# Kernel optimization log

Measured on AMD Instinct MI355X. Metric: run time of the kernel, lower is better.

Reference implementation:

```python
import jax, jax.numpy as jnp
import numpy as np
from jax import lax

C = 64
K = 7
HALF = K // 2
SIGMA_MIN = 0.6
SIGMA_MAX = 1.2

_SOBEL_X = jnp.array([[-1., 0., 1.], [-2., 0., 2.], [-1., 0., 1.]], dtype=jnp.float32).reshape(1, 1, 3, 3)
_SOBEL_Y = jnp.transpose(_SOBEL_X, (0, 1, 3, 2))


def _depthwise3x3(x, kern):
    # x: [B,C,H,W]; same 3x3 kernel per channel -> fold C into batch, 1-channel conv
    B, Cc, H, W = x.shape
    y = lax.conv_general_dilated(
        x.reshape(B * Cc, 1, H, W), kern,
        window_strides=(1, 1), padding=((1, 1), (1, 1)),
        dimension_numbers=('NCHW', 'OIHW', 'NCHW'))
    return y.reshape(B, Cc, H, W)


def _shift_stack(xp, W_out, axis):
    # xp padded by HALF along `axis`; stack K shifted views along new last axis
    views = [lax.slice_in_dim(xp, i, i + W_out, axis=axis) for i in range(K)]
    return jnp.stack(views, axis=-1)


def setup_inputs() -> dict:
    key = jax.random.key(0)
    x = jax.random.normal(key, (4, C, 256, 256), dtype=jnp.float32)
    return {"x": x}


def reference(x) -> jnp.ndarray:
    B, Cc, H, W = x.shape
    # Sobel edge magnitude, mean over channels
    gx = _depthwise3x3(x, _SOBEL_X)
    gy = _depthwise3x3(x, _SOBEL_Y)
    edge = (gx ** 2 + gy ** 2).mean(axis=1, keepdims=True)  # [B,1,H,W]
    emin = edge.min(axis=(2, 3), keepdims=True)
    emax = edge.max(axis=(2, 3), keepdims=True)
    edge = (edge - emin) / (emax + 1e-6)  # note: denom = amax + eps (faithful)
    sigma = SIGMA_MIN + (SIGMA_MAX - SIGMA_MIN) * edge  # [B,1,H,W]

    # per-pixel 1D gaussian kernel, shared across channels: [B,1,H,W,K]
    offs = jnp.arange(-HALF, HALF + 1, dtype=x.dtype)
    g = jnp.exp(-(offs ** 2) / (2.0 * sigma[..., None] ** 2))
    g = g / g.sum(axis=-1, keepdims=True)

    # horizontal pass: pad W, gather K shifted views, weighted sum
    xp = jnp.pad(x, ((0, 0), (0, 0), (0, 0), (HALF, HALF)))
    out = (_shift_stack(xp, W, axis=3) * g).sum(axis=-1)
    # vertical pass with the same per-pixel kernel
    op = jnp.pad(out, ((0, 0), (0, 0), (HALF, HALF), (0, 0)))
    out = (_shift_stack(op, H, axis=2) * g).sum(axis=-1)
    return out
```

## Files before the change

### kernel.cpp

```cpp
#include <hip/hip_runtime.h>
#include <cstddef>

namespace {
constexpr int B = 4, C = 64, H = 256, W = 256;
constexpr int HW = H * W;
constexpr int CHW = C * HW;
constexpr int CG = 4;
constexpr int TH = 16;
constexpr float SMIN = 0.6f, SMAX = 1.2f;
typedef float vfloat4 __attribute__((ext_vector_type(4)));
}

__device__ __forceinline__ float4 ld4(const float* p) {
  return *(const float4*)p;
}
__device__ __forceinline__ void st4(float* p, float a, float b, float c, float d) {
  float4 v; v.x = a; v.y = b; v.z = c; v.w = d; *(float4*)p = v;
}
__device__ __forceinline__ void st4nt(float* p, float a, float b, float c, float d) {
  vfloat4 v; v.x = a; v.y = b; v.z = c; v.w = d;
  __builtin_nontemporal_store(v, (vfloat4*)p);
}

__global__ __launch_bounds__(256) void edge_kernel(
    const float* __restrict__ x, float* __restrict__ P) {
  __shared__ float part[4][4][64][4];
  const int xcd = blockIdx.x & 7;
  const int slot = blockIdx.x >> 3;
  const int hbb = slot & 7;
  const int cb = slot >> 3;
  const int h0 = xcd * 32 + hbb * 4;
  const int cg = cb >> 2;
  const int b = cb & 3;
  const int lane = threadIdx.x & 63, wv = threadIdx.x >> 6;
  const float* base = x + (size_t)b * CHW + 4 * lane;
  const int c0 = cg * 16 + wv * 4;
  float acc[4][4] = {};
  #pragma unroll
  for (int cc = 0; cc < 4; ++cc) {
    const float* p = base + (size_t)(c0 + cc) * HW;
    float4 R[6];
    #pragma unroll
    for (int i = 0; i < 6; ++i) {
      const int gh = h0 - 1 + i;
      R[i] = (gh >= 0 && gh < H) ? ld4(p + (size_t)gh * W)
                                 : float4{0.f, 0.f, 0.f, 0.f};
    }
    float Lh[6], Rh[6];
    #pragma unroll
    for (int i = 0; i < 6; ++i) {
      Lh[i] = __shfl_up(R[i].w, 1);
      Rh[i] = __shfl_down(R[i].x, 1);
    }
    if (lane == 0) {
      #pragma unroll
      for (int i = 0; i < 6; ++i) Lh[i] = 0.f;
    }
    if (lane == 63) {
      #pragma unroll
      for (int i = 0; i < 6; ++i) Rh[i] = 0.f;
    }
    #pragma unroll
    for (int r = 0; r < 4; ++r) {
      const float ra[6] = {Lh[r],     R[r].x,     R[r].y,     R[r].z,     R[r].w,     Rh[r]};
      const float rb[6] = {Lh[r + 1], R[r + 1].x, R[r + 1].y, R[r + 1].z, R[r + 1].w, Rh[r + 1]};
      const float rc[6] = {Lh[r + 2], R[r + 2].x, R[r + 2].y, R[r + 2].z, R[r + 2].w, Rh[r + 2]};
      #pragma unroll
      for (int j = 0; j < 4; ++j) {
        float gx = (ra[j + 2] - ra[j]) + 2.f * (rb[j + 2] - rb[j]) + (rc[j + 2] - rc[j]);
        float gy = (rc[j] - ra[j]) + 2.f * (rc[j + 1] - ra[j + 1]) + (rc[j + 2] - ra[j + 2]);
        acc[r][j] = fmaf(gx, gx, acc[r][j]);
        acc[r][j] = fmaf(gy, gy, acc[r][j]);
      }
    }
  }
  #pragma unroll
  for (int r = 0; r < 4; ++r)
    #pragma unroll
    for (int j = 0; j < 4; ++j) part[wv][r][lane][j] = acc[r][j];
  __syncthreads();
  {
    const int r = wv;
    float s[4];
    #pragma unroll
    for (int j = 0; j < 4; ++j)
      s[j] = part[0][r][lane][j] + part[1][r][lane][j] +
             part[2][r][lane][j] + part[3][r][lane][j];
    st4nt(P + (size_t)(cg * B + b) * HW + (size_t)(h0 + r) * W + 4 * lane,
          s[0], s[1], s[2], s[3]);
  }
}

__global__ __launch_bounds__(256) void combine_kernel(
    const float* __restrict__ P, float* __restrict__ edge,
    float* __restrict__ mmp) {
  __shared__ float smn[4], smx[4];
  const int t = blockIdx.x * 256 + threadIdx.x;
  const int pix4 = t * 4;
  const int b = pix4 >> 16;
  const int off = pix4 & (HW - 1);
  float4 s0 = ld4(P + (size_t)(0 * B + b) * HW + off);
  float4 s1 = ld4(P + (size_t)(1 * B + b) * HW + off);
  float4 s2 = ld4(P + (size_t)(2 * B + b) * HW + off);
  float4 s3 = ld4(P + (size_t)(3 * B + b) * HW + off);
  float e0 = (s0.x + s1.x + s2.x + s3.x) * (1.f / 64.f);
  float e1 = (s0.y + s1.y + s2.y + s3.y) * (1.f / 64.f);
  float e2 = (s0.z + s1.z + s2.z + s3.z) * (1.f / 64.f);
  float e3 = (s0.w + s1.w + s2.w + s3.w) * (1.f / 64.f);
  st4(edge + pix4, e0, e1, e2, e3);
  float mn = fminf(fminf(e0, e1), fminf(e2, e3));
  float mx = fmaxf(fmaxf(e0, e1), fmaxf(e2, e3));
  #pragma unroll
  for (int o = 32; o > 0; o >>= 1) {
    mn = fminf(mn, __shfl_down(mn, o, 64));
    mx = fmaxf(mx, __shfl_down(mx, o, 64));
  }
  const int lane = threadIdx.x & 63, wv = threadIdx.x >> 6;
  if (lane == 0) { smn[wv] = mn; smx[wv] = mx; }
  __syncthreads();
  if (threadIdx.x == 0) {
    mn = fminf(fminf(smn[0], smn[1]), fminf(smn[2], smn[3]));
    mx = fmaxf(fmaxf(smx[0], smx[1]), fmaxf(smx[2], smx[3]));
    mmp[2 * (b * 64 + (blockIdx.x & 63))] = mn;
    mmp[2 * (b * 64 + (blockIdx.x & 63)) + 1] = mx;
  }
}

__global__ __launch_bounds__(256) void weights_kernel(
    const float* __restrict__ edge, const float* __restrict__ mmp,
    float* __restrict__ wt) {
  const int t = blockIdx.x * 256 + threadIdx.x;
  const int pix4 = t * 4;
  const int b = pix4 >> 16;
  const int lane = threadIdx.x & 63;
  float2 mv = *(const float2*)&mmp[2 * (b * 64 + lane)];
  float mn = mv.x, mx = mv.y;
  #pragma unroll
  for (int o = 1; o < 64; o <<= 1) {
    mn = fminf(mn, __shfl_xor(mn, o, 64));
    mx = fmaxf(mx, __shfl_xor(mx, o, 64));
  }
  const float emin = mn;
  const float inv_den = 1.f / (mx + 1e-6f);
  float4 ev = ld4(edge + pix4);
  const float E[4] = {ev.x, ev.y, ev.z, ev.w};
  float r[8];
  #pragma unroll
  for (int j = 0; j < 4; ++j) {
    float en = (E[j] - emin) * inv_den;
    float sg = SMIN + (SMAX - SMIN) * en;
    float a = 1.0f / (2.0f * sg * sg);
    float e1 = __expf(-a);
    float t2 = e1 * e1, e4 = t2 * t2, e9 = e4 * e4 * e1;
    float inv = 1.f / (1.f + 2.f * (e1 + e4 + e9));
    r[2 * j] = e1; r[2 * j + 1] = inv;
  }
  st4(wt + (size_t)pix4 * 2,     r[0], r[1], r[2], r[3]);
  st4(wt + (size_t)pix4 * 2 + 4, r[4], r[5], r[6], r[7]);
}

__device__ __forceinline__ void recon_g(float e1, float inv, float g[7]) {
  float t2 = e1 * e1, e4 = t2 * t2, e9 = e4 * e4 * e1;
  g[3] = inv; g[2] = e1 * inv; g[1] = e4 * inv; g[0] = e9 * inv;
  g[4] = g[2]; g[5] = g[1]; g[6] = g[0];
}

__global__ __launch_bounds__(256) void fusedblur_kernel(
    const float* __restrict__ x, const float* __restrict__ wt,
    float* __restrict__ out) {
  __shared__ float hb[TH + 6][W];
  const int xcd = blockIdx.x & 7;
  const int slot = blockIdx.x >> 3;
  const int s = slot & 15;
  const int bc = xcd * 32 + (slot >> 4);
  const int b = bc >> 6;
  const int h0 = s * TH;
  const int lane = threadIdx.x & 63, wv = threadIdx.x >> 6;
  const float* xp = x + (size_t)bc * HW + 4 * lane;
  const float* wp = wt + (size_t)b * HW * 2 + 8 * lane;
  float* op = out + (size_t)bc * HW + 4 * lane;

  for (int r = wv; r < TH + 6; r += 4) {
    const int gh = h0 - 3 + r;
    float4 o = {0.f, 0.f, 0.f, 0.f};
    if (gh >= 0 && gh < H) {
      float4 v = ld4(xp + (size_t)gh * W);
      float4 q0 = ld4(wp + (size_t)gh * W * 2);
      float4 q1 = ld4(wp + (size_t)gh * W * 2 + 4);
      float L1 = __shfl_up(v.y, 1), L2 = __shfl_up(v.z, 1), L3 = __shfl_up(v.w, 1);
      float R1 = __shfl_down(v.x, 1), R2 = __shfl_down(v.y, 1), R3 = __shfl_down(v.z, 1);
      if (lane == 0)  { L1 = 0.f; L2 = 0.f; L3 = 0.f; }
      if (lane == 63) { R1 = 0.f; R2 = 0.f; R3 = 0.f; }
      const float win[10] = {L1, L2, L3, v.x, v.y, v.z, v.w, R1, R2, R3};
      const float E1[4] = {q0.x, q0.z, q1.x, q1.z};
      const float IV[4] = {q0.y, q0.w, q1.y, q1.w};
      float acc[4];
      #pragma unroll
      for (int j = 0; j < 4; ++j) {
        float g[7]; recon_g(E1[j], IV[j], g);
        float sacc = g[0] * win[j];
        #pragma unroll
        for (int i = 1; i < 7; ++i) sacc = fmaf(g[i], win[j + i], sacc);
        acc[j] = sacc;
      }
      o.x = acc[0]; o.y = acc[1]; o.z = acc[2]; o.w = acc[3];
    }
    *(float4*)&hb[r][4 * lane] = o;
  }
  __syncthreads();

  const int r0 = wv * 4;
  float win7[7][4];
  #pragma unroll
  for (int i = 0; i < 7; ++i) {
    float4 v = *(const float4*)&hb[r0 + i][4 * lane];
    win7[i][0] = v.x; win7[i][1] = v.y; win7[i][2] = v.z; win7[i][3] = v.w;
  }
  #pragma unroll
  for (int k = 0; k < 4; ++k) {
    const int gh = h0 + r0 + k;
    float4 q0 = ld4(wp + (size_t)gh * W * 2);
    float4 q1 = ld4(wp + (size_t)gh * W * 2 + 4);
    const float E1[4] = {q0.x, q0.z, q1.x, q1.z};
    const float IV[4] = {q0.y, q0.w, q1.y, q1.w};
    float acc[4];
    #pragma unroll
    for (int j = 0; j < 4; ++j) {
      float g[7]; recon_g(E1[j], IV[j], g);
      float sacc = g[0] * win7[0][j];
      #pragma unroll
      for (int i = 1; i < 7; ++i) sacc = fmaf(g[i], win7[i][j], sacc);
      acc[j] = sacc;
    }
    st4nt(op + (size_t)gh * W, acc[0], acc[1], acc[2], acc[3]);
    if (k < 3) {
      #pragma unroll
      for (int i = 0; i < 6; ++i) {
        #pragma unroll
        for (int j = 0; j < 4; ++j) win7[i][j] = win7[i + 1][j];
      }
      float4 nv = *(const float4*)&hb[r0 + k + 7][4 * lane];
      win7[6][0] = nv.x; win7[6][1] = nv.y; win7[6][2] = nv.z; win7[6][3] = nv.w;
    }
  }
}

extern "C" void kernel_launch(void* const* d_in, const int* in_sizes, int n_in,
                              void* d_out, int out_size, void* d_ws, size_t ws_size,
                              hipStream_t stream) {
  const float* x = (const float*)d_in[0];
  float* out = (float*)d_out;

  float* mmp = (float*)d_ws;
  float* edge = (float*)((char*)d_ws + 4096);
  float* wt = (float*)((char*)d_ws + 4096 + (size_t)B * HW * 4);
  float* P = (float*)((char*)d_ws + 4096 + (size_t)B * HW * 12);

  edge_kernel<<<B * CG * (H / 4), 256, 0, stream>>>(x, P);
  combine_kernel<<<(B * HW / 4) / 256, 256, 0, stream>>>(P, edge, mmp);
  weights_kernel<<<(B * HW / 4) / 256, 256, 0, stream>>>(edge, mmp, wt);
  fusedblur_kernel<<<B * C * (H / TH), 256, 0, stream>>>(x, wt, out);
}
```

Baseline: 134.7 us.

## Fuse combine and weights kernels with atomic grid-wide min/max barrier

```diff
diff --git a/kernel.cpp b/kernel.cpp
--- a/kernel.cpp
+++ b/kernel.cpp
@@ -5,7 +5,8 @@
 constexpr int B = 4, C = 64, H = 256, W = 256;
 constexpr int HW = H * W;
 constexpr int CHW = C * HW;
-constexpr int CG = 4;
+constexpr int CG = 8;
+constexpr int BH = 8;
 constexpr int TH = 16;
 constexpr float SMIN = 0.6f, SMAX = 1.2f;
 typedef float vfloat4 __attribute__((ext_vector_type(4)));
@@ -21,47 +22,54 @@
   vfloat4 v; v.x = a; v.y = b; v.z = c; v.w = d;
   __builtin_nontemporal_store(v, (vfloat4*)p);
 }
+__device__ __forceinline__ float4 ld4nt(const float* p) {
+  vfloat4 v = __builtin_nontemporal_load((const vfloat4*)p);
+  float4 r; r.x = v.x; r.y = v.y; r.z = v.z; r.w = v.w; return r;
+}
 
 __global__ __launch_bounds__(256) void edge_kernel(
-    const float* __restrict__ x, float* __restrict__ P) {
-  __shared__ float part[4][4][64][4];
+    const float* __restrict__ x, float* __restrict__ P,
+    unsigned int* __restrict__ mm) {
+  __shared__ float part[4][BH][64][4];
+  if (blockIdx.x == 0 && threadIdx.x < 2 * B + 1)
+    mm[threadIdx.x] = (threadIdx.x < B) ? 0x7f7fffffu : 0u;
   const int xcd = blockIdx.x & 7;
   const int slot = blockIdx.x >> 3;
-  const int hbb = slot & 7;
-  const int cb = slot >> 3;
-  const int h0 = xcd * 32 + hbb * 4;
+  const int hbb = slot & 3;
+  const int cb = slot >> 2;
+  const int h0 = xcd * 32 + hbb * BH;
   const int cg = cb >> 2;
   const int b = cb & 3;
   const int lane = threadIdx.x & 63, wv = threadIdx.x >> 6;
   const float* base = x + (size_t)b * CHW + 4 * lane;
-  const int c0 = cg * 16 + wv * 4;
-  float acc[4][4] = {};
-  #pragma unroll
-  for (int cc = 0; cc < 4; ++cc) {
+  const int c0 = cg * 8 + wv * 2;
+  float acc[BH][4] = {};
+  #pragma unroll
+  for (int cc = 0; cc < 2; ++cc) {
     const float* p = base + (size_t)(c0 + cc) * HW;
-    float4 R[6];
-    #pragma unroll
-    for (int i = 0; i < 6; ++i) {
+    float4 R[BH + 2];
+    #pragma unroll
+    for (int i = 0; i < BH + 2; ++i) {
       const int gh = h0 - 1 + i;
       R[i] = (gh >= 0 && gh < H) ? ld4(p + (size_t)gh * W)
                                  : float4{0.f, 0.f, 0.f, 0.f};
     }
-    float Lh[6], Rh[6];
-    #pragma unroll
-    for (int i = 0; i < 6; ++i) {
+    float Lh[BH + 2], Rh[BH + 2];
+    #pragma unroll
+    for (int i = 0; i < BH + 2; ++i) {
       Lh[i] = __shfl_up(R[i].w, 1);
       Rh[i] = __shfl_down(R[i].x, 1);
     }
     if (lane == 0) {
       #pragma unroll
-      for (int i = 0; i < 6; ++i) Lh[i] = 0.f;
+      for (int i = 0; i < BH + 2; ++i) Lh[i] = 0.f;
     }
     if (lane == 63) {
       #pragma unroll
-      for (int i = 0; i < 6; ++i) Rh[i] = 0.f;
-    }
-    #pragma unroll
-    for (int r = 0; r < 4; ++r) {
+      for (int i = 0; i < BH + 2; ++i) Rh[i] = 0.f;
+    }
+    #pragma unroll
+    for (int r = 0; r < BH; ++r) {
       const float ra[6] = {Lh[r],     R[r].x,     R[r].y,     R[r].z,     R[r].w,     Rh[r]};
       const float rb[6] = {Lh[r + 1], R[r + 1].x, R[r + 1].y, R[r + 1].z, R[r + 1].w, Rh[r + 1]};
       const float rc[6] = {Lh[r + 2], R[r + 2].x, R[r + 2].y, R[r + 2].z, R[r + 2].w, Rh[r + 2]};
@@ -75,12 +83,13 @@
     }
   }
   #pragma unroll
-  for (int r = 0; r < 4; ++r)
+  for (int r = 0; r < BH; ++r)
     #pragma unroll
     for (int j = 0; j < 4; ++j) part[wv][r][lane][j] = acc[r][j];
   __syncthreads();
-  {
-    const int r = wv;
+  #pragma unroll
+  for (int rr = 0; rr < 2; ++rr) {
+    const int r = wv + 4 * rr;
     float s[4];
     #pragma unroll
     for (int j = 0; j < 4; ++j)
@@ -91,25 +100,25 @@
   }
 }
 
-__global__ __launch_bounds__(256) void combine_kernel(
-    const float* __restrict__ P, float* __restrict__ edge,
-    float* __restrict__ mmp) {
+__global__ __launch_bounds__(256) void combine_weights_kernel(
+    const float* __restrict__ P, unsigned int* __restrict__ mm,
+    float* __restrict__ wt) {
   __shared__ float smn[4], smx[4];
+  __shared__ unsigned int sld[2];
   const int t = blockIdx.x * 256 + threadIdx.x;
   const int pix4 = t * 4;
   const int b = pix4 >> 16;
   const int off = pix4 & (HW - 1);
-  float4 s0 = ld4(P + (size_t)(0 * B + b) * HW + off);
-  float4 s1 = ld4(P + (size_t)(1 * B + b) * HW + off);
-  float4 s2 = ld4(P + (size_t)(2 * B + b) * HW + off);
-  float4 s3 = ld4(P + (size_t)(3 * B + b) * HW + off);
-  float e0 = (s0.x + s1.x + s2.x + s3.x) * (1.f / 64.f);
-  float e1 = (s0.y + s1.y + s2.y + s3.y) * (1.f / 64.f);
-  float e2 = (s0.z + s1.z + s2.z + s3.z) * (1.f / 64.f);
-  float e3 = (s0.w + s1.w + s2.w + s3.w) * (1.f / 64.f);
-  st4(edge + pix4, e0, e1, e2, e3);
-  float mn = fminf(fminf(e0, e1), fminf(e2, e3));
-  float mx = fmaxf(fmaxf(e0, e1), fmaxf(e2, e3));
+  float e[4] = {};
+  #pragma unroll
+  for (int g = 0; g < CG; ++g) {
+    float4 sv = ld4nt(P + (size_t)(g * B + b) * HW + off);
+    e[0] += sv.x; e[1] += sv.y; e[2] += sv.z; e[3] += sv.w;
+  }
+  #pragma unroll
+  for (int j = 0; j < 4; ++j) e[j] *= (1.f / 64.f);
+  float mn = fminf(fminf(e[0], e[1]), fminf(e[2], e[3]));
+  float mx = fmaxf(fmaxf(e[0], e[1]), fmaxf(e[2], e[3]));
   #pragma unroll
   for (int o = 32; o > 0; o >>= 1) {
     mn = fminf(mn, __shfl_down(mn, o, 64));
@@ -121,33 +130,23 @@
   if (threadIdx.x == 0) {
     mn = fminf(fminf(smn[0], smn[1]), fminf(smn[2], smn[3]));
     mx = fmaxf(fmaxf(smx[0], smx[1]), fmaxf(smx[2], smx[3]));
-    mmp[2 * (b * 64 + (blockIdx.x & 63))] = mn;
-    mmp[2 * (b * 64 + (blockIdx.x & 63)) + 1] = mx;
-  }
-}
-
-__global__ __launch_bounds__(256) void weights_kernel(
-    const float* __restrict__ edge, const float* __restrict__ mmp,
-    float* __restrict__ wt) {
-  const int t = blockIdx.x * 256 + threadIdx.x;
-  const int pix4 = t * 4;
-  const int b = pix4 >> 16;
-  const int lane = threadIdx.x & 63;
-  float2 mv = *(const float2*)&mmp[2 * (b * 64 + lane)];
-  float mn = mv.x, mx = mv.y;
-  #pragma unroll
-  for (int o = 1; o < 64; o <<= 1) {
-    mn = fminf(mn, __shfl_xor(mn, o, 64));
-    mx = fmaxf(mx, __shfl_xor(mx, o, 64));
-  }
-  const float emin = mn;
-  const float inv_den = 1.f / (mx + 1e-6f);
-  float4 ev = ld4(edge + pix4);
-  const float E[4] = {ev.x, ev.y, ev.z, ev.w};
+    atomicMin(mm + b, __float_as_uint(mn));
+    atomicMax(mm + B + b, __float_as_uint(mx));
+    __threadfence();
+    atomicAdd(mm + 2 * B, 1u);
+    while (__hip_atomic_load(mm + 2 * B, __ATOMIC_ACQUIRE,
+                             __HIP_MEMORY_SCOPE_AGENT) < gridDim.x)
+      __builtin_amdgcn_s_sleep(2);
+    sld[0] = __hip_atomic_load(mm + b, __ATOMIC_ACQUIRE, __HIP_MEMORY_SCOPE_AGENT);
+    sld[1] = __hip_atomic_load(mm + B + b, __ATOMIC_ACQUIRE, __HIP_MEMORY_SCOPE_AGENT);
+  }
+  __syncthreads();
+  const float emin = __uint_as_float(sld[0]);
+  const float inv_den = 1.f / (__uint_as_float(sld[1]) + 1e-6f);
   float r[8];
   #pragma unroll
   for (int j = 0; j < 4; ++j) {
-    float en = (E[j] - emin) * inv_den;
+    float en = (e[j] - emin) * inv_den;
     float sg = SMIN + (SMAX - SMIN) * en;
     float a = 1.0f / (2.0f * sg * sg);
     float e1 = __expf(-a);
@@ -251,13 +250,11 @@
   const float* x = (const float*)d_in[0];
   float* out = (float*)d_out;
 
-  float* mmp = (float*)d_ws;
-  float* edge = (float*)((char*)d_ws + 4096);
-  float* wt = (float*)((char*)d_ws + 4096 + (size_t)B * HW * 4);
-  float* P = (float*)((char*)d_ws + 4096 + (size_t)B * HW * 12);
-
-  edge_kernel<<<B * CG * (H / 4), 256, 0, stream>>>(x, P);
-  combine_kernel<<<(B * HW / 4) / 256, 256, 0, stream>>>(P, edge, mmp);
-  weights_kernel<<<(B * HW / 4) / 256, 256, 0, stream>>>(edge, mmp, wt);
+  unsigned int* mm = (unsigned int*)d_ws;
+  float* wt = (float*)((char*)d_ws + 4096);
+  float* P = (float*)((char*)d_ws + 4096 + (size_t)B * HW * 8);
+
+  edge_kernel<<<B * CG * (H / BH), 256, 0, stream>>>(x, P, mm);
+  combine_weights_kernel<<<(B * HW / 4) / 256, 256, 0, stream>>>(P, mm, wt);
   fusedblur_kernel<<<B * C * (H / TH), 256, 0, stream>>>(x, wt, out);
 }
```

Result: slower. 150.5 us (+11.8%).
